# Optimization experiments

Hardware: AMD Instinct MI355X
Metric: run time of the kernel (lower is better)

## Reference

```python
import jax, jax.numpy as jnp
import numpy as np

LAMBDA_K_TAU = 0.1
RIDGE = 0.1


def _masked_cov(x, mask, counts):
    """Covariance of masked rows. x: [B,S,D], mask: [B,S] float, counts: [B] float.
    Equivalent to packing the masked rows (batch_2d_tensor) then _torch_cov."""
    xm = x * mask[..., None]
    mean = xm.sum(axis=1) / counts[:, None]                 # [B,D]
    xc = (xm - mean[:, None, :]) * mask[..., None]          # [B,S,D]
    cov = jnp.einsum('bsi,bsj->bij', xc, xc)
    return cov / (counts - 1.0)[:, None, None]


def _calc_label_cov_inv(task_cov, label_cov):
    d = task_cov.shape[-1]
    eye = jnp.eye(d, dtype=task_cov.dtype)
    return jnp.linalg.inv(LAMBDA_K_TAU * label_cov + (1.0 - LAMBDA_K_TAU) * task_cov + RIDGE * eye)


def setup_inputs() -> dict:
    key = jax.random.key(0)
    ks = jax.random.split(key, 6)
    B, S, Q, D = 256, 512, 256, 512
    support_set = jax.random.normal(ks[0], (B, S, D), dtype=jnp.float32)
    support_labels = jax.random.randint(ks[1], (B, S), 0, 2, dtype=jnp.int32)
    query_set = jax.random.normal(ks[2], (B, Q, D), dtype=jnp.float32)
    # lengths in [len//2, len] so both classes are present and counts > 1
    support_set_lengths = jax.random.randint(ks[3], (B,), S // 2, S + 1, dtype=jnp.int32)
    query_set_lengths = jax.random.randint(ks[4], (B,), Q // 2, Q + 1, dtype=jnp.int32)
    log_prediction_scaling = jnp.asarray(np.log(10.0), dtype=jnp.float32)
    return {
        'support_set': support_set,
        'support_labels': support_labels,
        'query_set': query_set,
        'support_set_lengths': support_set_lengths,
        'query_set_lengths': query_set_lengths,
        'log_prediction_scaling': log_prediction_scaling,
    }


def reference(support_set, support_labels, query_set, support_set_lengths,
              query_set_lengths, log_prediction_scaling):
    B, S, D = support_set.shape
    Q = query_set.shape[1]
    f32 = support_set.dtype

    sup_valid = (jnp.arange(S)[None, :] < support_set_lengths[:, None]).astype(f32)  # [B,S]
    mask_pos = (support_labels == 1).astype(f32) * sup_valid                          # [B,S]
    mask_neg = (support_labels == 0).astype(f32) * sup_valid

    pos_counts = mask_pos.sum(axis=1)   # [B]
    neg_counts = mask_neg.sum(axis=1)
    sup_counts = support_set_lengths.astype(f32)

    positive_mean = jnp.einsum('bsd,bs->bd', support_set, mask_pos) / pos_counts[:, None]
    negative_mean = jnp.einsum('bsd,bs->bd', support_set, mask_neg) / neg_counts[:, None]

    cov_mats = _masked_cov(support_set, sup_valid, sup_counts)   # task covariance
    pos_mats = _masked_cov(support_set, mask_pos, pos_counts)    # == cov of packed positives
    neg_mats = _masked_cov(support_set, mask_neg, neg_counts)

    pos_inv = _calc_label_cov_inv(cov_mats, pos_mats)  # [B,D,D]
    neg_inv = _calc_label_cov_inv(cov_mats, neg_mats)

    q_valid = (jnp.arange(Q)[None, :] < query_set_lengths[:, None]).astype(f32)  # [B,Q]

    pos_diff = positive_mean[:, None, :] - query_set  # [B,Q,D]
    neg_diff = negative_mean[:, None, :] - query_set
    pos_maha = jnp.einsum('bik,bkx,bix->bi', pos_diff, pos_inv, pos_diff) * q_valid
    neg_maha = jnp.einsum('bik,bkx,bix->bi', neg_diff, neg_inv, neg_diff) * q_valid

    logit_scale = jnp.exp(log_prediction_scaling)
    # scale is applied inside batch_calculate_mahalanobis_logits AND again in forward
    logits = jnp.stack([neg_maha, pos_maha], axis=-1) * (-1.0) * logit_scale
    return logits * logit_scale  # [B,Q,2]
```

## Files before the change

kernel.cpp:

```cpp
#include <hip/hip_runtime.h>
#include <hip/hip_bf16.h>

#define TPB 256
constexpr int B_ = 256, S_ = 512, D_ = 512, Q_ = 256, NM_ = 512;
constexpr int NB = 64, NT = 8;

typedef _Float16 f16x8 __attribute__((ext_vector_type(8)));
typedef float f32x4 __attribute__((ext_vector_type(4)));

__device__ __forceinline__ void decode_mt(int bid, int W, int& m, int& t){
  int x = bid & 7, r = bid >> 3;
  t = r % W; int u = r / W;
  m = (((u >> 1)*8 + x) << 1) | (u & 1);
}

__device__ __forceinline__ void stage_D(const float* __restrict__ src, size_t ld,
                                        float (*dst)[68], int t)
{
  int r = t >> 2, seg = (t & 3) * 16;
  const float4* s4 = (const float4*)(src + (size_t)r*ld + seg);
  #pragma unroll
  for (int i=0;i<4;i++) *((float4*)&dst[r][seg + i*4]) = s4[i];
}

__device__ __forceinline__ void mm_acc68(const float (*Aop)[68], const float (*Bop)[68],
                                         float acc[4][4], int tr, int tc)
{
  for (int kk=0;kk<64;kk++){
    float4 av = *((const float4*)&Aop[kk][tr*4]);
    float4 bv = *((const float4*)&Bop[kk][tc*4]);
    float a[4]={av.x,av.y,av.z,av.w}, b2[4]={bv.x,bv.y,bv.z,bv.w};
    #pragma unroll
    for (int u=0;u<4;u++)
      #pragma unroll
      for (int v=0;v<4;v++) acc[u][v] = fmaf(a[u], b2[v], acc[u][v]);
  }
}

__global__ __launch_bounds__(TPB) void k_stats(const float* __restrict__ X,
                                               const int* __restrict__ labels,
                                               const int* __restrict__ slen,
                                               float* __restrict__ mu,
                                               float* __restrict__ cnt,
                                               unsigned int* __restrict__ wpbits)
{
  int b = blockIdx.x, t = threadIdx.x;
  __shared__ int lab[S_];
  __shared__ float red[TPB];
  int L = slen[b];
  for (int s = t; s < S_; s += TPB) {
    int lb = labels[b*S_ + s];
    lab[s] = (s < L) ? lb : -1;
  }
  __syncthreads();
  if (t < 16) {
    unsigned int wword = 0;
    for (int i2 = 0; i2 < 32; i2++) if (lab[t*32 + i2] == 1) wword |= (1u << i2);
    wpbits[b*16 + t] = wword;
  }
  int cpi=0, cni=0;
  for (int s=t; s<S_; s+=TPB){ cpi += (lab[s]==1); cni += (lab[s]==0); }
  red[t] = (float)cpi; __syncthreads();
  for (int o=TPB/2;o>0;o>>=1){ if(t<o) red[t]+=red[t+o]; __syncthreads(); }
  float cp = red[0]; __syncthreads();
  red[t] = (float)cni; __syncthreads();
  for (int o=TPB/2;o>0;o>>=1){ if(t<o) red[t]+=red[t+o]; __syncthreads(); }
  float cn = red[0];
  if (t==0){ cnt[b*2+0]=cn; cnt[b*2+1]=cp; }
  float sp0=0,sp1=0,sn0=0,sn1=0;
  const float* Xb = X + (size_t)b*S_*D_;
  for (int s=0;s<S_;s++){
    int e = lab[s];
    if (e < 0) continue;
    float x0 = Xb[(size_t)s*D_ + t];
    float x1 = Xb[(size_t)s*D_ + t + 256];
    if (e==1){ sp0+=x0; sp1+=x1; } else { sn0+=x0; sn1+=x1; }
  }
  float stv = (float)L;
  float* mb = mu + (size_t)b*3*D_;
  mb[0*D_ + t] = sn0/cn;        mb[0*D_ + t+256] = sn1/cn;
  mb[1*D_ + t] = sp0/cp;        mb[1*D_ + t+256] = sp1/cp;
  mb[2*D_ + t] = (sn0+sp0)/stv; mb[2*D_ + t+256] = (sn1+sp1)/stv;
}

__global__ __launch_bounds__(TPB) void k_prep(const float* __restrict__ X,
                                              const int* __restrict__ slen,
                                              unsigned short* __restrict__ Xvh,
                                              unsigned short* __restrict__ Xvl)
{
  int b = blockIdx.y, z = blockIdx.x;
  int d0 = (z>>3)*64, s0 = (z&7)*64;
  int t = threadIdx.x;
  __shared__ float Tl[64][65];
  const float* src = X + ((size_t)b*S_ + s0)*D_ + d0;
  { int r = t>>2, seg = (t&3)*16;
    const float4* s4 = (const float4*)(src + (size_t)r*D_ + seg);
    #pragma unroll
    for (int i=0;i<4;i++){ float4 v = s4[i];
      Tl[seg+i*4+0][r]=v.x; Tl[seg+i*4+1][r]=v.y; Tl[seg+i*4+2][r]=v.z; Tl[seg+i*4+3][r]=v.w; } }
  __syncthreads();
  int L = slen[b];
  int dr = t>>2, sc = (t&3)*16;
  union U16 { unsigned short u[8]; uint4 v; };
  U16 H[2], Lo[2];
  #pragma unroll
  for (int g=0; g<2; g++)
    #pragma unroll
    for (int i=0;i<8;i++){
      int si = sc + g*8 + i;
      float x = (s0+si < L) ? Tl[dr][si] : 0.f;
      _Float16 hh = (_Float16)x;
      float lo = x - (float)hh;
      H[g].u[i]  = __builtin_bit_cast(unsigned short, hh);
      Lo[g].u[i] = __builtin_bit_cast(unsigned short, (_Float16)lo);
    }
  size_t o = ((size_t)b*D_ + d0+dr)*S_ + s0 + sc;
  *(uint4*)(Xvh+o)   = H[0].v;  *(uint4*)(Xvh+o+8) = H[1].v;
  *(uint4*)(Xvl+o)   = Lo[0].v; *(uint4*)(Xvl+o+8) = Lo[1].v;
}

__global__ __launch_bounds__(TPB,2) void k_gram(const unsigned short* __restrict__ Xvh,
                                                const unsigned short* __restrict__ Xvl,
                                                const unsigned int* __restrict__ wpbits,
                                                const float* __restrict__ mu,
                                                const float* __restrict__ cnt,
                                                const int* __restrict__ slen,
                                                float* __restrict__ A)
{
  __shared__ unsigned short sAvh[128][32], sAvl[128][32], sAph[128][32], sApl[128][32],
                            sBvh[128][32], sBvl[128][32];
  int id = blockIdx.x;
  int g = id>>3;
  int b = (g/10)*8 + (id&7);
  int z = g%10;
  int ti=0; while (z >= 4-ti){ z -= 4-ti; ti++; } int tj = ti + z;
  int i0 = ti*128, j0 = tj*128;
  int t = threadIdx.x, lane = t&63, w = t>>6;
  int wr = w>>1, wc = w&1, l15 = lane&15;

  f32x4 acc_t[4][4], acc_p[4][4];
  f32x4 z4 = {0.f,0.f,0.f,0.f};
  #pragma unroll
  for (int mf=0;mf<4;mf++)
    #pragma unroll
    for (int nf=0;nf<4;nf++){ acc_t[mf][nf]=z4; acc_p[mf][nf]=z4; }

  const size_t baseA = ((size_t)b*D_ + i0)*S_;
  const size_t baseB = ((size_t)b*D_ + j0)*S_;
  int phx = (lane>>4) ^ ((l15>>1)&3);

  for (int ks=0; ks<16; ks++){
    int s0 = ks*32;
    unsigned int wpw = wpbits[b*16 + ks];
    __syncthreads();
    #pragma unroll
    for (int h=0; h<2; h++){
      int ci = t + h*256;
      int row = ci>>2, cpos = ci&3;
      int ph = cpos ^ ((row>>1)&3);
      size_t ga = baseA + (size_t)row*S_ + s0 + cpos*8;
      size_t gb = baseB + (size_t)row*S_ + s0 + cpos*8;
      uint4 vh = *(const uint4*)(Xvh+ga);
      uint4 vl = *(const uint4*)(Xvl+ga);
      uint4 bh = *(const uint4*)(Xvh+gb);
      uint4 bl = *(const uint4*)(Xvl+gb);
      unsigned int m8 = (wpw >> (cpos*8)) & 0xFFu;
      uint4 mk;
      mk.x = ((m8&1u)?0xFFFFu:0u)  | ((m8&2u)?0xFFFF0000u:0u);
      mk.y = ((m8&4u)?0xFFFFu:0u)  | ((m8&8u)?0xFFFF0000u:0u);
      mk.z = ((m8&16u)?0xFFFFu:0u) | ((m8&32u)?0xFFFF0000u:0u);
      mk.w = ((m8&64u)?0xFFFFu:0u) | ((m8&128u)?0xFFFF0000u:0u);
      uint4 p4, q4;
      p4.x = vh.x&mk.x; p4.y = vh.y&mk.y; p4.z = vh.z&mk.z; p4.w = vh.w&mk.w;
      q4.x = vl.x&mk.x; q4.y = vl.y&mk.y; q4.z = vl.z&mk.z; q4.w = vl.w&mk.w;
      *(uint4*)&sAvh[row][ph*8] = vh;
      *(uint4*)&sAvl[row][ph*8] = vl;
      *(uint4*)&sAph[row][ph*8] = p4;
      *(uint4*)&sApl[row][ph*8] = q4;
      *(uint4*)&sBvh[row][ph*8] = bh;
      *(uint4*)&sBvl[row][ph*8] = bl;
    }
    __syncthreads();
    f16x8 Avh[4], Avl[4], Aph[4], Apl[4];
    #pragma unroll
    for (int mf=0;mf<4;mf++){
      int r = wr*64 + mf*16 + l15;
      Avh[mf] = __builtin_bit_cast(f16x8, *(const uint4*)&sAvh[r][phx*8]);
      Avl[mf] = __builtin_bit_cast(f16x8, *(const uint4*)&sAvl[r][phx*8]);
      Aph[mf] = __builtin_bit_cast(f16x8, *(const uint4*)&sAph[r][phx*8]);
      Apl[mf] = __builtin_bit_cast(f16x8, *(const uint4*)&sApl[r][phx*8]);
    }
    #pragma unroll
    for (int nf=0;nf<4;nf++){
      int r = wc*64 + nf*16 + l15;
      f16x8 Bh = __builtin_bit_cast(f16x8, *(const uint4*)&sBvh[r][phx*8]);
      f16x8 Bl = __builtin_bit_cast(f16x8, *(const uint4*)&sBvl[r][phx*8]);
      #pragma unroll
      for (int mf=0;mf<4;mf++){
        acc_t[mf][nf] = __builtin_amdgcn_mfma_f32_16x16x32_f16(Avh[mf], Bh, acc_t[mf][nf],0,0,0);
        acc_t[mf][nf] = __builtin_amdgcn_mfma_f32_16x16x32_f16(Avh[mf], Bl, acc_t[mf][nf],0,0,0);
        acc_t[mf][nf] = __builtin_amdgcn_mfma_f32_16x16x32_f16(Avl[mf], Bh, acc_t[mf][nf],0,0,0);
        acc_p[mf][nf] = __builtin_amdgcn_mfma_f32_16x16x32_f16(Aph[mf], Bh, acc_p[mf][nf],0,0,0);
        acc_p[mf][nf] = __builtin_amdgcn_mfma_f32_16x16x32_f16(Aph[mf], Bl, acc_p[mf][nf],0,0,0);
        acc_p[mf][nf] = __builtin_amdgcn_mfma_f32_16x16x32_f16(Apl[mf], Bh, acc_p[mf][nf],0,0,0);
      }
    }
  }
  float cn = cnt[b*2+0], cp = cnt[b*2+1];
  float stv = (float)slen[b];
  float kn = 0.1f/(cn-1.f), kp = 0.1f/(cp-1.f), kt = 0.9f/(stv-1.f);
  float rn = 0.1f*cn/(cn-1.f), rp = 0.1f*cp/(cp-1.f), rt = 0.9f*stv/(stv-1.f);
  const float* mb = mu + (size_t)b*3*D_;
  float* A0 = A + (size_t)(b*2+0)*D_*D_;
  float* A1 = A + (size_t)(b*2+1)*D_*D_;
  int rbase = i0 + wr*64 + (lane>>4)*4;
  int cbase = j0 + wc*64 + l15;
  #pragma unroll
  for (int mf=0;mf<4;mf++){
    #pragma unroll
    for (int i=0;i<4;i++){
      int r = rbase + mf*16 + i;
      float mnr = mb[r], mpr = mb[D_+r], mtr = mb[2*D_+r];
      #pragma unroll
      for (int nf=0;nf<4;nf++){
        int c = cbase + nf*16;
        float mnc = mb[c], mpc = mb[D_+c], mtc = mb[2*D_+c];
        float gp = acc_p[mf][nf][i];
        float gt = acc_t[mf][nf][i];
        float gn = gt - gp;
        float diag = (r==c)?0.1f:0.f;
        A0[(size_t)r*D_ + c] = kn*gn + kt*gt - rn*mnr*mnc - rt*mtr*mtc + diag;
        A1[(size_t)r*D_ + c] = kp*gp + kt*gt - rp*mpr*mpc - rt*mtr*mtc + diag;
      }
    }
  }
}

__global__ __launch_bounds__(TPB) void k_diag(float* __restrict__ A,
                                              float* __restrict__ invDT, int j)
{
  int m, t0; decode_mt(blockIdx.x, 1, m, t0); (void)t0;
  int t = threadIdx.x;
  __shared__ float Ld[64][65];
  __shared__ float Iv[64][65];
  float* Ab = A + (size_t)m*D_*D_ + (size_t)(j*NB)*D_ + j*NB;
  for (int l=t; l<4096; l+=TPB){ int r=l>>6, c=l&63; Ld[r][c] = Ab[(size_t)r*D_ + c]; Iv[r][c] = 0.f; }
  __syncthreads();
  for (int k=0;k<64;k++){
    if (t==0) Ld[k][k] = sqrtf(Ld[k][k]);
    __syncthreads();
    if (t>k && t<64) Ld[t][k] /= Ld[k][k];
    __syncthreads();
    for (int l=t; l<4096; l+=TPB){
      int r=l>>6, c=l&63;
      if (r>k && c>k) Ld[r][c] = fmaf(-Ld[r][k], Ld[c][k], Ld[r][c]);
    }
    __syncthreads();
  }
  if (t < 64){
    int c = t;
    Iv[c][c] = 1.f/Ld[c][c];
    for (int r=c+1;r<64;r++){
      float s = 0.f;
      for (int k2=c;k2<r;k2++) s += Ld[r][k2]*Iv[k2][c];
      Iv[r][c] = -s/Ld[r][r];
    }
  }
  __syncthreads();
  float* Ib = invDT + ((size_t)m*8 + j)*4096;
  for (int l=t; l<4096; l+=TPB){ Ib[l] = Iv[l&63][l>>6]; }
}

__global__ __launch_bounds__(TPB) void k_panel(float* __restrict__ A,
                                               const float* __restrict__ invDT,
                                               int j, int W)
{
  int m, ti; decode_mt(blockIdx.x, W, m, ti);
  int ib = j + 1 + ti;
  int t = threadIdx.x, tr = t&15, tc = t>>4;
  __shared__ float Ta[64][68], Tb[64][68];
  float* U = A + (size_t)m*D_*D_ + (size_t)(j*NB)*D_ + ib*NB;
  stage_D(invDT + ((size_t)m*8 + j)*4096, 64, Ta, t);
  stage_D(U, D_, Tb, t);
  __syncthreads();
  float acc[4][4] = {};
  mm_acc68(Ta, Tb, acc, tr, tc);
  #pragma unroll
  for (int u=0;u<4;u++){
    float4 o = make_float4(acc[u][0],acc[u][1],acc[u][2],acc[u][3]);
    *((float4*)(U + (size_t)(tr*4+u)*D_ + tc*4)) = o;
  }
}

__global__ __launch_bounds__(TPB) void k_trailrow(float* __restrict__ A, int j, int row, int W)
{
  int m, z; decode_mt(blockIdx.x, W, m, z);
  int b2 = row + z;
  int t = threadIdx.x, tr = t&15, tc = t>>4;
  __shared__ float Ta[64][68], Tb[64][68];
  float* Am = A + (size_t)m*D_*D_;
  stage_D(Am + (size_t)(j*NB)*D_ + row*NB, D_, Ta, t);
  stage_D(Am + (size_t)(j*NB)*D_ + b2*NB, D_, Tb, t);
  __syncthreads();
  float acc[4][4] = {};
  mm_acc68(Ta, Tb, acc, tr, tc);
  float* Cb = Am + (size_t)(row*NB)*D_ + b2*NB;
  #pragma unroll
  for (int u=0;u<4;u++){
    float4* pC = (float4*)(Cb + (size_t)(tr*4+u)*D_ + tc*4);
    float4 o = *pC;
    o.x -= acc[u][0]; o.y -= acc[u][1]; o.z -= acc[u][2]; o.w -= acc[u][3];
    *pC = o;
  }
}

__global__ __launch_bounds__(TPB) void k_trail2(float* __restrict__ A, int jb, int W)
{
  int m, z; decode_mt(blockIdx.x, W, m, z);
  int base = jb + 2;
  int Tn = NT - base;
  int p = 0, zz = z;
  while (zz >= Tn - p){ zz -= Tn - p; p++; }
  int a2 = base + p, b2 = a2 + zz;
  int t = threadIdx.x, tr = t&15, tc = t>>4;
  __shared__ float Ta[64][68], Tb[64][68];
  float* Am = A + (size_t)m*D_*D_;
  float acc[4][4] = {};
  stage_D(Am + (size_t)(jb*NB)*D_ + a2*NB, D_, Ta, t);
  stage_D(Am + (size_t)(jb*NB)*D_ + b2*NB, D_, Tb, t);
  __syncthreads();
  mm_acc68(Ta, Tb, acc, tr, tc);
  __syncthreads();
  stage_D(Am + (size_t)((jb+1)*NB)*D_ + a2*NB, D_, Ta, t);
  stage_D(Am + (size_t)((jb+1)*NB)*D_ + b2*NB, D_, Tb, t);
  __syncthreads();
  mm_acc68(Ta, Tb, acc, tr, tc);
  float* Cb = Am + (size_t)(a2*NB)*D_ + b2*NB;
  #pragma unroll
  for (int u=0;u<4;u++){
    float4* pC = (float4*)(Cb + (size_t)(tr*4+u)*D_ + tc*4);
    float4 o = *pC;
    o.x -= acc[u][0]; o.y -= acc[u][1]; o.z -= acc[u][2]; o.w -= acc[u][3];
    *pC = o;
  }
}

__global__ __launch_bounds__(TPB) void k_solvefin(const float* __restrict__ Qs,
                                                  const float* __restrict__ mu,
                                                  const float* __restrict__ A,
                                                  const float* __restrict__ invDT,
                                                  float* __restrict__ Z,
                                                  const int* __restrict__ qlen,
                                                  const float* __restrict__ lps,
                                                  float* __restrict__ out)
{
  int m, t0; decode_mt(blockIdx.x, 4, m, t0);
  int q0 = t0*NB;
  int b = m>>1, cls = m&1;
  int t = threadIdx.x, tr = t&15, tc = t>>4;
  __shared__ float Ta[64][68], Tb[64][68];
  const float* Am = A + (size_t)m*D_*D_;
  float* Zm = Z + (size_t)m*D_*Q_;
  const float* muv = mu + ((size_t)b*3 + cls)*D_;
  float cs[4] = {0.f,0.f,0.f,0.f};
  for (int j=0;j<NT;j++){
    float acc[4][4];
    {
      float4 mv = *(const float4*)&muv[j*NB + tr*4];
      #pragma unroll
      for (int v=0;v<4;v++){
        float4 qv = *(const float4*)&Qs[((size_t)b*Q_ + q0 + tc*4 + v)*D_ + j*NB + tr*4];
        acc[0][v] = mv.x - qv.x;
        acc[1][v] = mv.y - qv.y;
        acc[2][v] = mv.z - qv.z;
        acc[3][v] = mv.w - qv.w;
      }
    }
    for (int k=0;k<j;k++){
      stage_D(Am + (size_t)(k*NB)*D_ + j*NB, D_, Ta, t);
      { int r = t >> 2, seg = (t & 3)*16;
        const float4* s4 = (const float4*)(Zm + (size_t)(k*NB + r)*Q_ + q0 + seg);
        #pragma unroll
        for (int i=0;i<4;i++) *((float4*)&Tb[r][seg + i*4]) = s4[i];
      }
      __syncthreads();
      for (int kk=0;kk<64;kk++){
        float4 av = *((const float4*)&Ta[kk][tr*4]);
        float4 bv = *((const float4*)&Tb[kk][tc*4]);
        float a[4]={av.x,av.y,av.z,av.w}, bb2[4]={bv.x,bv.y,bv.z,bv.w};
        #pragma unroll
        for (int u=0;u<4;u++)
          #pragma unroll
          for (int v=0;v<4;v++) acc[u][v] = fmaf(-a[u], bb2[v], acc[u][v]);
      }
      __syncthreads();
    }
    #pragma unroll
    for (int u=0;u<4;u++)
      #pragma unroll
      for (int v=0;v<4;v++) Tb[tr*4+u][tc*4+v] = acc[u][v];
    stage_D(invDT + ((size_t)m*8 + j)*4096, 64, Ta, t);
    __syncthreads();
    float o4[4][4] = {};
    for (int kk=0;kk<64;kk++){
      float4 av = *((const float4*)&Ta[kk][tr*4]);
      float4 bv = *((const float4*)&Tb[kk][tc*4]);
      float a[4]={av.x,av.y,av.z,av.w}, bb2[4]={bv.x,bv.y,bv.z,bv.w};
      #pragma unroll
      for (int u=0;u<4;u++)
        #pragma unroll
        for (int v=0;v<4;v++) o4[u][v] = fmaf(a[u], bb2[v], o4[u][v]);
    }
    if (j < NT-1){
      #pragma unroll
      for (int u=0;u<4;u++){
        float4 o = make_float4(o4[u][0], o4[u][1], o4[u][2], o4[u][3]);
        *((float4*)(Zm + (size_t)(j*NB + tr*4+u)*Q_ + q0 + tc*4)) = o;
      }
    }
    #pragma unroll
    for (int u=0;u<4;u++)
      #pragma unroll
      for (int v=0;v<4;v++) cs[v] = fmaf(o4[u][v], o4[u][v], cs[v]);
    __syncthreads();
  }
  float* red = &Ta[0][0];
  #pragma unroll
  for (int v=0;v<4;v++) red[(tc*4+v)*16 + tr] = cs[v];
  __syncthreads();
  if (t < 64){
    float s = 0.f;
    #pragma unroll
    for (int i=0;i<16;i++) s += red[t*16 + i];
    int q = q0 + t;
    float valid = (q < qlen[b]) ? 1.f : 0.f;
    float s2 = expf(2.f*lps[0]);
    out[((size_t)b*Q_ + q)*2 + cls] = -s2*s*valid;
  }
}

extern "C" void kernel_launch(void* const* d_in, const int* in_sizes, int n_in,
                              void* d_out, int out_size, void* d_ws, size_t ws_size,
                              hipStream_t stream) {
  (void)in_sizes; (void)n_in; (void)out_size;
  const float* X   = (const float*)d_in[0];
  const int*   lab = (const int*)d_in[1];
  const float* Qs  = (const float*)d_in[2];
  const int*   sl  = (const int*)d_in[3];
  const int*   ql  = (const int*)d_in[4];
  const float* lps = (const float*)d_in[5];
  float* out = (float*)d_out;

  float* A  = (float*)d_ws;
  float* Z  = A + (size_t)NM_*D_*D_;
  unsigned short* Xvh = (unsigned short*)Z;
  unsigned short* Xvl = Xvh + (size_t)B_*D_*S_;
  float* invDT = Z + (size_t)NM_*D_*Q_;
  float* mu   = invDT + (size_t)NM_*8*64*64;
  float* cnt  = mu + (size_t)B_*3*D_;
  unsigned int* wpbits = (unsigned int*)(cnt + B_*2);
  size_t need = (size_t)((char*)(wpbits + B_*16) - (char*)d_ws);
  if (ws_size < need) return;

  k_stats<<<dim3(B_), dim3(TPB), 0, stream>>>(X, lab, sl, mu, cnt, wpbits);
  k_prep<<<dim3(64, B_), dim3(TPB), 0, stream>>>(X, sl, Xvh, Xvl);
  k_gram<<<dim3(2560), dim3(TPB), 0, stream>>>(Xvh, Xvl, wpbits, mu, cnt, sl, A);

  for (int j=0; j<NT; j+=2){
    k_diag<<<dim3(NM_), dim3(TPB), 0, stream>>>(A, invDT, j);
    int nb0 = NT-1-j;
    if (nb0 > 0){
      k_panel<<<dim3(NM_*nb0), dim3(TPB), 0, stream>>>(A, invDT, j, nb0);
      int wr = NT - (j+1);
      k_trailrow<<<dim3(NM_*wr), dim3(TPB), 0, stream>>>(A, j, j+1, wr);
      k_diag<<<dim3(NM_), dim3(TPB), 0, stream>>>(A, invDT, j+1);
      int nb1 = NT-1-(j+1);
      if (nb1 > 0){
        k_panel<<<dim3(NM_*nb1), dim3(TPB), 0, stream>>>(A, invDT, j+1, nb1);
        int Tn = NT - (j+2);
        int np = Tn*(Tn+1)/2;
        if (np > 0) k_trail2<<<dim3(NM_*np), dim3(TPB), 0, stream>>>(A, j, np);
      }
    }
  }

  k_solvefin<<<dim3(NM_*4), dim3(TPB), 0, stream>>>(Qs, mu, A, invDT, Z, ql, lps, out);
}
```

Baseline: 2.657 ms.

## Use split-fp16 MFMA for Cholesky trailing updates and widen stats kernel

The panel kernel now also writes each solved panel tile as transposed high/low fp16 pairs into a packed scratch buffer. The trailing-update kernels read those pairs and compute the rank-64 updates with 16x16x32 fp16 MFMA using a three-term split product, replacing the scalar fp32 FMA loops. The stats kernel moves to 1024 threads so four groups split the support rows, with a shared-memory reduction at the end. This trades some precision and extra panel stores for matrix-core throughput; the Ut buffer reuses the Z/Xv workspace region.

After: 2.445 ms. -8.0%, faster.

```diff
diff --git a/kernel.cpp b/kernel.cpp
--- a/kernel.cpp
+++ b/kernel.cpp
@@ -7,6 +7,8 @@
 
 typedef _Float16 f16x8 __attribute__((ext_vector_type(8)));
 typedef float f32x4 __attribute__((ext_vector_type(4)));
+
+__device__ __forceinline__ int pidx(int j, int a){ return j*(15-j)/2 + (a-j-1); }
 
 __device__ __forceinline__ void decode_mt(int bid, int W, int& m, int& t){
   int x = bid & 7, r = bid >> 3;
@@ -37,20 +39,22 @@
   }
 }
 
-__global__ __launch_bounds__(TPB) void k_stats(const float* __restrict__ X,
-                                               const int* __restrict__ labels,
-                                               const int* __restrict__ slen,
-                                               float* __restrict__ mu,
-                                               float* __restrict__ cnt,
-                                               unsigned int* __restrict__ wpbits)
+__global__ __launch_bounds__(1024) void k_stats(const float* __restrict__ X,
+                                                const int* __restrict__ labels,
+                                                const int* __restrict__ slen,
+                                                float* __restrict__ mu,
+                                                float* __restrict__ cnt,
+                                                unsigned int* __restrict__ wpbits)
 {
   int b = blockIdx.x, t = threadIdx.x;
+  int td = t & 255, sg = t >> 8;
   __shared__ int lab[S_];
-  __shared__ float red[TPB];
+  __shared__ float red[1024];
+  __shared__ float part[4][256][4];
   int L = slen[b];
-  for (int s = t; s < S_; s += TPB) {
-    int lb = labels[b*S_ + s];
-    lab[s] = (s < L) ? lb : -1;
+  if (t < S_) {
+    int lb = labels[b*S_ + t];
+    lab[t] = (t < L) ? lb : -1;
   }
   __syncthreads();
   if (t < 16) {
@@ -58,29 +62,36 @@
     for (int i2 = 0; i2 < 32; i2++) if (lab[t*32 + i2] == 1) wword |= (1u << i2);
     wpbits[b*16 + t] = wword;
   }
-  int cpi=0, cni=0;
-  for (int s=t; s<S_; s+=TPB){ cpi += (lab[s]==1); cni += (lab[s]==0); }
-  red[t] = (float)cpi; __syncthreads();
-  for (int o=TPB/2;o>0;o>>=1){ if(t<o) red[t]+=red[t+o]; __syncthreads(); }
+  red[t] = (t < S_) ? ((lab[t]==1) ? 1.f : 0.f) : 0.f;
+  __syncthreads();
+  for (int o=512;o>0;o>>=1){ if(t<o) red[t]+=red[t+o]; __syncthreads(); }
   float cp = red[0]; __syncthreads();
-  red[t] = (float)cni; __syncthreads();
-  for (int o=TPB/2;o>0;o>>=1){ if(t<o) red[t]+=red[t+o]; __syncthreads(); }
+  red[t] = (t < S_) ? ((lab[t]==0) ? 1.f : 0.f) : 0.f;
+  __syncthreads();
+  for (int o=512;o>0;o>>=1){ if(t<o) red[t]+=red[t+o]; __syncthreads(); }
   float cn = red[0];
   if (t==0){ cnt[b*2+0]=cn; cnt[b*2+1]=cp; }
   float sp0=0,sp1=0,sn0=0,sn1=0;
   const float* Xb = X + (size_t)b*S_*D_;
-  for (int s=0;s<S_;s++){
+  for (int s=sg*128; s<sg*128+128; s++){
     int e = lab[s];
     if (e < 0) continue;
-    float x0 = Xb[(size_t)s*D_ + t];
-    float x1 = Xb[(size_t)s*D_ + t + 256];
+    float x0 = Xb[(size_t)s*D_ + td];
+    float x1 = Xb[(size_t)s*D_ + td + 256];
     if (e==1){ sp0+=x0; sp1+=x1; } else { sn0+=x0; sn1+=x1; }
   }
-  float stv = (float)L;
-  float* mb = mu + (size_t)b*3*D_;
-  mb[0*D_ + t] = sn0/cn;        mb[0*D_ + t+256] = sn1/cn;
-  mb[1*D_ + t] = sp0/cp;        mb[1*D_ + t+256] = sp1/cp;
-  mb[2*D_ + t] = (sn0+sp0)/stv; mb[2*D_ + t+256] = (sn1+sp1)/stv;
+  part[sg][td][0]=sn0; part[sg][td][1]=sn1; part[sg][td][2]=sp0; part[sg][td][3]=sp1;
+  __syncthreads();
+  if (sg == 0){
+    float a0=0,a1=0,a2=0,a3=0;
+    #pragma unroll
+    for (int g=0;g<4;g++){ a0+=part[g][td][0]; a1+=part[g][td][1]; a2+=part[g][td][2]; a3+=part[g][td][3]; }
+    float stv = (float)L;
+    float* mb = mu + (size_t)b*3*D_;
+    mb[0*D_ + td] = a0/cn;      mb[0*D_ + td+256] = a1/cn;
+    mb[1*D_ + td] = a2/cp;      mb[1*D_ + td+256] = a3/cp;
+    mb[2*D_ + td] = (a0+a2)/stv; mb[2*D_ + td+256] = (a1+a3)/stv;
+  }
 }
 
 __global__ __launch_bounds__(TPB) void k_prep(const float* __restrict__ X,
@@ -273,6 +284,7 @@
 
 __global__ __launch_bounds__(TPB) void k_panel(float* __restrict__ A,
                                                const float* __restrict__ invDT,
+                                               unsigned short* __restrict__ Ut,
                                                int j, int W)
 {
   int m, ti; decode_mt(blockIdx.x, W, m, ti);
@@ -290,31 +302,100 @@
     float4 o = make_float4(acc[u][0],acc[u][1],acc[u][2],acc[u][3]);
     *((float4*)(U + (size_t)(tr*4+u)*D_ + tc*4)) = o;
   }
-}
-
-__global__ __launch_bounds__(TPB) void k_trailrow(float* __restrict__ A, int j, int row, int W)
+  __syncthreads();
+  unsigned short* shh = (unsigned short*)Ta;
+  unsigned short* shl = (unsigned short*)Tb;
+  #pragma unroll
+  for (int u=0;u<4;u++)
+    #pragma unroll
+    for (int v=0;v<4;v++){
+      float val = acc[u][v];
+      _Float16 h = (_Float16)val;
+      float lo = val - (float)h;
+      shh[(tc*4+v)*72 + tr*4+u] = __builtin_bit_cast(unsigned short, h);
+      shl[(tc*4+v)*72 + tr*4+u] = __builtin_bit_cast(unsigned short, (_Float16)lo);
+    }
+  __syncthreads();
+  unsigned short* Ub = Ut + ((size_t)m*28 + pidx(j, ib)) * 8192;
+  { int r = t>>2, cs = (t&3)*16;
+    *(uint4*)(Ub + r*64 + cs)          = *(uint4*)&shh[r*72 + cs];
+    *(uint4*)(Ub + r*64 + cs + 8)      = *(uint4*)&shh[r*72 + cs + 8];
+    *(uint4*)(Ub + 4096 + r*64 + cs)   = *(uint4*)&shl[r*72 + cs];
+    *(uint4*)(Ub + 4096 + r*64 + cs+8) = *(uint4*)&shl[r*72 + cs + 8];
+  }
+}
+
+__device__ __forceinline__ void trail_stage(const unsigned short* __restrict__ Ua,
+                                            const unsigned short* __restrict__ Ub,
+                                            unsigned short (*Ah)[72], unsigned short (*Al)[72],
+                                            unsigned short (*Bh)[72], unsigned short (*Bl)[72],
+                                            int t)
+{
+  int r = t>>2, cs = (t&3)*16;
+  *(uint4*)&Ah[r][cs]   = *(const uint4*)(Ua + r*64 + cs);
+  *(uint4*)&Ah[r][cs+8] = *(const uint4*)(Ua + r*64 + cs + 8);
+  *(uint4*)&Al[r][cs]   = *(const uint4*)(Ua + 4096 + r*64 + cs);
+  *(uint4*)&Al[r][cs+8] = *(const uint4*)(Ua + 4096 + r*64 + cs + 8);
+  *(uint4*)&Bh[r][cs]   = *(const uint4*)(Ub + r*64 + cs);
+  *(uint4*)&Bh[r][cs+8] = *(const uint4*)(Ub + r*64 + cs + 8);
+  *(uint4*)&Bl[r][cs]   = *(const uint4*)(Ub + 4096 + r*64 + cs);
+  *(uint4*)&Bl[r][cs+8] = *(const uint4*)(Ub + 4096 + r*64 + cs + 8);
+}
+
+__device__ __forceinline__ void trail_mfma(const unsigned short (*Ah)[72], const unsigned short (*Al)[72],
+                                           const unsigned short (*Bh)[72], const unsigned short (*Bl)[72],
+                                           f32x4 acc[4], int w, int l15, int lk)
+{
+  #pragma unroll
+  for (int s=0;s<2;s++){
+    f16x8 Afh = __builtin_bit_cast(f16x8, *(const uint4*)&Ah[w*16 + l15][s*32 + lk*8]);
+    f16x8 Afl = __builtin_bit_cast(f16x8, *(const uint4*)&Al[w*16 + l15][s*32 + lk*8]);
+    #pragma unroll
+    for (int ni=0;ni<4;ni++){
+      f16x8 Bfh = __builtin_bit_cast(f16x8, *(const uint4*)&Bh[ni*16 + l15][s*32 + lk*8]);
+      f16x8 Bfl = __builtin_bit_cast(f16x8, *(const uint4*)&Bl[ni*16 + l15][s*32 + lk*8]);
+      acc[ni] = __builtin_amdgcn_mfma_f32_16x16x32_f16(Afh, Bfh, acc[ni],0,0,0);
+      acc[ni] = __builtin_amdgcn_mfma_f32_16x16x32_f16(Afh, Bfl, acc[ni],0,0,0);
+      acc[ni] = __builtin_amdgcn_mfma_f32_16x16x32_f16(Afl, Bfh, acc[ni],0,0,0);
+    }
+  }
+}
+
+__device__ __forceinline__ void trail_rmw(float* __restrict__ Cb, const f32x4 acc[4],
+                                          int w, int l15, int lk)
+{
+  #pragma unroll
+  for (int ni=0;ni<4;ni++)
+    #pragma unroll
+    for (int i=0;i<4;i++){
+      int r = w*16 + lk*4 + i, cc = ni*16 + l15;
+      float* pC = Cb + (size_t)r*D_ + cc;
+      *pC -= acc[ni][i];
+    }
+}
+
+__global__ __launch_bounds__(TPB) void k_trailrow(float* __restrict__ A,
+                                                  const unsigned short* __restrict__ Ut,
+                                                  int j, int row, int W)
 {
   int m, z; decode_mt(blockIdx.x, W, m, z);
   int b2 = row + z;
-  int t = threadIdx.x, tr = t&15, tc = t>>4;
-  __shared__ float Ta[64][68], Tb[64][68];
-  float* Am = A + (size_t)m*D_*D_;
-  stage_D(Am + (size_t)(j*NB)*D_ + row*NB, D_, Ta, t);
-  stage_D(Am + (size_t)(j*NB)*D_ + b2*NB, D_, Tb, t);
-  __syncthreads();
-  float acc[4][4] = {};
-  mm_acc68(Ta, Tb, acc, tr, tc);
-  float* Cb = Am + (size_t)(row*NB)*D_ + b2*NB;
-  #pragma unroll
-  for (int u=0;u<4;u++){
-    float4* pC = (float4*)(Cb + (size_t)(tr*4+u)*D_ + tc*4);
-    float4 o = *pC;
-    o.x -= acc[u][0]; o.y -= acc[u][1]; o.z -= acc[u][2]; o.w -= acc[u][3];
-    *pC = o;
-  }
-}
-
-__global__ __launch_bounds__(TPB) void k_trail2(float* __restrict__ A, int jb, int W)
+  int t = threadIdx.x, lane = t&63, w = t>>6, l15 = lane&15, lk = lane>>4;
+  __shared__ unsigned short Ah[64][72], Al[64][72], Bh[64][72], Bl[64][72];
+  const unsigned short* Um = Ut + (size_t)m*28*8192;
+  trail_stage(Um + (size_t)pidx(j,row)*8192, Um + (size_t)pidx(j,b2)*8192, Ah, Al, Bh, Bl, t);
+  __syncthreads();
+  f32x4 acc[4];
+  #pragma unroll
+  for (int ni=0;ni<4;ni++) acc[ni] = (f32x4){0.f,0.f,0.f,0.f};
+  trail_mfma(Ah, Al, Bh, Bl, acc, w, l15, lk);
+  float* Cb = A + (size_t)m*D_*D_ + (size_t)(row*NB)*D_ + b2*NB;
+  trail_rmw(Cb, acc, w, l15, lk);
+}
+
+__global__ __launch_bounds__(TPB) void k_trail2(float* __restrict__ A,
+                                                const unsigned short* __restrict__ Ut,
+                                                int jb, int W)
 {
   int m, z; decode_mt(blockIdx.x, W, m, z);
   int base = jb + 2;
@@ -322,27 +403,22 @@
   int p = 0, zz = z;
   while (zz >= Tn - p){ zz -= Tn - p; p++; }
   int a2 = base + p, b2 = a2 + zz;
-  int t = threadIdx.x, tr = t&15, tc = t>>4;
-  __shared__ float Ta[64][68], Tb[64][68];
-  float* Am = A + (size_t)m*D_*D_;
-  float acc[4][4] = {};
-  stage_D(Am + (size_t)(jb*NB)*D_ + a2*NB, D_, Ta, t);
-  stage_D(Am + (size_t)(jb*NB)*D_ + b2*NB, D_, Tb, t);
-  __syncthreads();
-  mm_acc68(Ta, Tb, acc, tr, tc);
-  __syncthreads();
-  stage_D(Am + (size_t)((jb+1)*NB)*D_ + a2*NB, D_, Ta, t);
-  stage_D(Am + (size_t)((jb+1)*NB)*D_ + b2*NB, D_, Tb, t);
-  __syncthreads();
-  mm_acc68(Ta, Tb, acc, tr, tc);
-  float* Cb = Am + (size_t)(a2*NB)*D_ + b2*NB;
-  #pragma unroll
-  for (int u=0;u<4;u++){
-    float4* pC = (float4*)(Cb + (size_t)(tr*4+u)*D_ + tc*4);
-    float4 o = *pC;
-    o.x -= acc[u][0]; o.y -= acc[u][1]; o.z -= acc[u][2]; o.w -= acc[u][3];
-    *pC = o;
-  }
+  int t = threadIdx.x, lane = t&63, w = t>>6, l15 = lane&15, lk = lane>>4;
+  __shared__ unsigned short Ah[64][72], Al[64][72], Bh[64][72], Bl[64][72];
+  const unsigned short* Um = Ut + (size_t)m*28*8192;
+  f32x4 acc[4];
+  #pragma unroll
+  for (int ni=0;ni<4;ni++) acc[ni] = (f32x4){0.f,0.f,0.f,0.f};
+  #pragma unroll
+  for (int c=0;c<2;c++){
+    int j = jb + c;
+    __syncthreads();
+    trail_stage(Um + (size_t)pidx(j,a2)*8192, Um + (size_t)pidx(j,b2)*8192, Ah, Al, Bh, Bl, t);
+    __syncthreads();
+    trail_mfma(Ah, Al, Bh, Bl, acc, w, l15, lk);
+  }
+  float* Cb = A + (size_t)m*D_*D_ + (size_t)(a2*NB)*D_ + b2*NB;
+  trail_rmw(Cb, acc, w, l15, lk);
 }
 
 __global__ __launch_bounds__(TPB) void k_solvefin(const float* __restrict__ Qs,
@@ -455,6 +531,7 @@
   float* Z  = A + (size_t)NM_*D_*D_;
   unsigned short* Xvh = (unsigned short*)Z;
   unsigned short* Xvl = Xvh + (size_t)B_*D_*S_;
+  unsigned short* Ut  = (unsigned short*)Z;
   float* invDT = Z + (size_t)NM_*D_*Q_;
   float* mu   = invDT + (size_t)NM_*8*64*64;
   float* cnt  = mu + (size_t)B_*3*D_;
@@ -462,7 +539,7 @@
   size_t need = (size_t)((char*)(wpbits + B_*16) - (char*)d_ws);
   if (ws_size < need) return;
 
-  k_stats<<<dim3(B_), dim3(TPB), 0, stream>>>(X, lab, sl, mu, cnt, wpbits);
+  k_stats<<<dim3(B_), dim3(1024), 0, stream>>>(X, lab, sl, mu, cnt, wpbits);
   k_prep<<<dim3(64, B_), dim3(TPB), 0, stream>>>(X, sl, Xvh, Xvl);
   k_gram<<<dim3(2560), dim3(TPB), 0, stream>>>(Xvh, Xvl, wpbits, mu, cnt, sl, A);
 
@@ -470,16 +547,16 @@
     k_diag<<<dim3(NM_), dim3(TPB), 0, stream>>>(A, invDT, j);
     int nb0 = NT-1-j;
     if (nb0 > 0){
-      k_panel<<<dim3(NM_*nb0), dim3(TPB), 0, stream>>>(A, invDT, j, nb0);
+      k_panel<<<dim3(NM_*nb0), dim3(TPB), 0, stream>>>(A, invDT, Ut, j, nb0);
       int wr = NT - (j+1);
-      k_trailrow<<<dim3(NM_*wr), dim3(TPB), 0, stream>>>(A, j, j+1, wr);
+      k_trailrow<<<dim3(NM_*wr), dim3(TPB), 0, stream>>>(A, Ut, j, j+1, wr);
       k_diag<<<dim3(NM_), dim3(TPB), 0, stream>>>(A, invDT, j+1);
       int nb1 = NT-1-(j+1);
       if (nb1 > 0){
-        k_panel<<<dim3(NM_*nb1), dim3(TPB), 0, stream>>>(A, invDT, j+1, nb1);
+        k_panel<<<dim3(NM_*nb1), dim3(TPB), 0, stream>>>(A, invDT, Ut, j+1, nb1);
         int Tn = NT - (j+2);
         int np = Tn*(Tn+1)/2;
-        if (np > 0) k_trail2<<<dim3(NM_*np), dim3(TPB), 0, stream>>>(A, j, np);
+        if (np > 0) k_trail2<<<dim3(NM_*np), dim3(TPB), 0, stream>>>(A, Ut, j, np);
       }
     }
   }
```
